# Performance work log

Measured on AMD Instinct MI355X. Metric: run time of the kernel, lower is better.

The kernel has to match this reference:

```python
import jax, jax.numpy as jnp
import numpy as np

N_MASTER = 100000
N_BOND = 200000
N_GLOB = 5000
E1 = 400000
E2 = 100000
D_IN = 64
D_OUT = 64
H = 4
SLOPE = 0.2  # leaky relu negative slope


def _mlp(x, W0, b0, W1, b1, W2):
    # LinearN with num_fc_layers=3: ELU, ELU, Identity (last layer no bias)
    h = jax.nn.elu(x @ W0 + b0)
    h = jax.nn.elu(h @ W1 + b1)
    return h @ W2  # (N, H*D_OUT)


def setup_inputs() -> dict:
    key = jax.random.key(0)
    ks = jax.random.split(key, 32)
    s = 0.1  # weight scale
    d = {
        "master_feats": jax.random.normal(ks[0], (N_MASTER, D_IN), jnp.float32),
        "bond_feats": jax.random.normal(ks[1], (N_BOND, D_IN), jnp.float32),
        "global_feats": jax.random.normal(ks[2], (N_GLOB, D_IN), jnp.float32),
        "atom_W0": jax.random.normal(ks[3], (D_IN, D_OUT), jnp.float32) * s,
        "atom_b0": jnp.zeros((D_OUT,), jnp.float32),
        "atom_W1": jax.random.normal(ks[4], (D_OUT, D_OUT), jnp.float32) * s,
        "atom_b1": jnp.zeros((D_OUT,), jnp.float32),
        "atom_W2": jax.random.normal(ks[5], (D_OUT, H * D_OUT), jnp.float32) * s,
        "bond_W0": jax.random.normal(ks[6], (D_IN, D_OUT), jnp.float32) * s,
        "bond_b0": jnp.zeros((D_OUT,), jnp.float32),
        "bond_W1": jax.random.normal(ks[7], (D_OUT, D_OUT), jnp.float32) * s,
        "bond_b1": jnp.zeros((D_OUT,), jnp.float32),
        "bond_W2": jax.random.normal(ks[8], (D_OUT, H * D_OUT), jnp.float32) * s,
        "glob_W0": jax.random.normal(ks[9], (D_IN, D_OUT), jnp.float32) * s,
        "glob_b0": jnp.zeros((D_OUT,), jnp.float32),
        "glob_W1": jax.random.normal(ks[10], (D_OUT, D_OUT), jnp.float32) * s,
        "glob_b1": jnp.zeros((D_OUT,), jnp.float32),
        "glob_W2": jax.random.normal(ks[11], (D_OUT, H * D_OUT), jnp.float32) * s,
        "attn_l": jax.random.normal(ks[12], (H, D_OUT), jnp.float32) * s,
        "attn_r": jax.random.normal(ks[13], (H, D_OUT), jnp.float32) * s,
        "e1_src": jax.random.randint(ks[14], (E1,), 0, N_BOND, jnp.int32),
        "e1_dst": jax.random.randint(ks[15], (E1,), 0, N_MASTER, jnp.int32),
        "e2_src": jax.random.randint(ks[16], (E2,), 0, N_GLOB, jnp.int32),
        "e2_dst": jax.random.randint(ks[17], (E2,), 0, N_MASTER, jnp.int32),
    }
    return d


def reference(master_feats, bond_feats, global_feats,
              atom_W0, atom_b0, atom_W1, atom_b1, atom_W2,
              bond_W0, bond_b0, bond_W1, bond_b1, bond_W2,
              glob_W0, glob_b0, glob_W1, glob_b1, glob_W2,
              attn_l, attn_r, e1_src, e1_dst, e2_src, e2_dst):
    # Per-node-type projections to (N, H, D_OUT)
    ft_m = _mlp(master_feats, atom_W0, atom_b0, atom_W1, atom_b1, atom_W2).reshape(N_MASTER, H, D_OUT)
    ft_b = _mlp(bond_feats, bond_W0, bond_b0, bond_W1, bond_b1, bond_W2).reshape(N_BOND, H, D_OUT)
    ft_g = _mlp(global_feats, glob_W0, glob_b0, glob_W1, glob_b1, glob_W2).reshape(N_GLOB, H, D_OUT)

    er = jnp.einsum('nhd,hd->nh', ft_m, attn_r)  # master (dst) scores
    el_b = jnp.einsum('nhd,hd->nh', ft_b, attn_l)
    el_g = jnp.einsum('nhd,hd->nh', ft_g, attn_l)

    # Per-edge logits: u_add_v then leaky relu
    e1 = jax.nn.leaky_relu(el_b[e1_src] + er[e1_dst], negative_slope=SLOPE)  # (E1, H)
    e2 = jax.nn.leaky_relu(el_g[e2_src] + er[e2_dst], negative_slope=SLOPE)  # (E2, H)

    # Joint edge softmax over all incoming edges per master node
    dst_all = jnp.concatenate([e1_dst, e2_dst])  # (E1+E2,)
    e_all = jnp.concatenate([e1, e2], axis=0)    # (E1+E2, H)
    emax = jax.ops.segment_max(e_all, dst_all, num_segments=N_MASTER)  # (N, H)
    ex = jnp.exp(e_all - emax[dst_all])
    esum = jax.ops.segment_sum(ex, dst_all, num_segments=N_MASTER)     # (N, H)
    a = ex / esum[dst_all]                                             # (E, H)

    # Aggregate: u_mul_e, sum per destination master node
    src_ft = jnp.concatenate([ft_b[e1_src], ft_g[e2_src]], axis=0)     # (E, H, D)
    msgs = src_ft * a[:, :, None]
    rst = jax.ops.segment_sum(msgs, dst_all, num_segments=N_MASTER)    # (N, H, D)
    return rst
```

## Files before the change

### kernel.cpp

```cpp
#include <hip/hip_runtime.h>

#define NM 100000
#define NB 200000
#define NG 5000
#define NE1 400000
#define NE2 100000
#define NE (NE1 + NE2)
#define NMP 100004
#define SCAN_BLOCKS 391

typedef __attribute__((ext_vector_type(8))) short bf16x8;
typedef __attribute__((ext_vector_type(4))) short short4v;
typedef __attribute__((ext_vector_type(4))) float f32x4;

__device__ __forceinline__ unsigned short f2bf(float f) {
    unsigned int u = __float_as_uint(f);
    u += 0x7FFFu + ((u >> 16) & 1u);
    return (unsigned short)(u >> 16);
}
__device__ __forceinline__ float bf2f(unsigned short u) {
    return __uint_as_float((unsigned int)u << 16);
}
__device__ __forceinline__ float elu_f(float x) {
    return x > 0.f ? x : __expf(x) - 1.f;
}
__device__ __forceinline__ char* swz(char* base, int j, int byteoff) {
    return base + j * 128 + ((((byteoff >> 4) ^ (j & 7)) << 4) | (byteoff & 15));
}

struct WEnt { const float* W; short* o; int I; int off; };
struct WAll { WEnt e[6]; };

__global__ __launch_bounds__(256) void wprep_all_kernel(WAll a)
{
    const int idx = blockIdx.x * 256 + threadIdx.x;
    #pragma unroll
    for (int j = 5; j >= 0; --j) {
        if (idx >= a.e[j].off) {
            const int local = idx - a.e[j].off;
            const int I = a.e[j].I;
            const int i = local >> 6, k = local & 63;
            a.e[j].o[local] = (short)f2bf(a.e[j].W[k * I + i]);
            break;
        }
    }
}

__global__ __launch_bounds__(256) void wt2prep_kernel(
    const float* __restrict__ W2b, const float* __restrict__ W2g,
    short* __restrict__ wt2)
{
    const int idx = blockIdx.x * 256 + threadIdx.x;
    const int i = idx >> 7, k = idx & 127;
    const float v = (k < 64) ? W2b[(k << 8) + i] : W2g[((k - 64) << 8) + i];
    wt2[idx] = (short)f2bf(v);
}

struct Eff3 { const float* W2[3]; const float* attn[3]; float* eff[3]; };
__global__ __launch_bounds__(256) void eff3_kernel(Eff3 a)
{
    const int b = blockIdx.x;
    const int t = threadIdx.x;
    const int h = t >> 6, k = t & 63;
    const float* wrow = a.W2[b] + (k << 8) + (h << 6);
    const float* arow = a.attn[b] + (h << 6);
    float s = 0.f;
    #pragma unroll 8
    for (int d = 0; d < 64; ++d) s = fmaf(wrow[d], arow[d], s);
    a.eff[b][(h << 6) + k] = s;
}

struct MlpArgs {
    const float* x[3]; int N[3];
    const short* W0t[3]; const float* b0[3];
    const short* W1t[3]; const float* b1[3];
    const float* eff[3];
    float* score[3];
    unsigned short* h2o[3];
    int bstart[3];
};

__global__ __launch_bounds__(256, 4) void mlp2_all_kernel(MlpArgs A)
{
    __shared__ __attribute__((aligned(128))) char ldsA[64 * 128];
    __shared__ __attribute__((aligned(128))) char ldsB[64 * 128];

    const int which = (blockIdx.x >= (unsigned)A.bstart[2]) ? 2
                    : (blockIdx.x >= (unsigned)A.bstart[1]) ? 1 : 0;
    const float* x = A.x[which];
    const int N = A.N[which];
    const short* W0t = A.W0t[which];
    const float* b0p = A.b0[which];
    const short* W1t = A.W1t[which];
    const float* b1p = A.b1[which];
    const float* eff = A.eff[which];
    float* score = A.score[which];
    unsigned short* h2p = A.h2o[which];

    const int tid = threadIdx.x;
    const int w = tid >> 6, l = tid & 63;
    const int g = l >> 4, c = l & 15;
    const int r0 = (blockIdx.x - A.bstart[which]) << 6;

    {
        const int j = tid >> 2, q = tid & 3;
        const int row = r0 + j;
        bf16x8 o0 = (bf16x8)0, o1 = (bf16x8)0;
        if (row < N) {
            const float4* xp = (const float4*)(x + ((size_t)row << 6) + (q << 4));
            #pragma unroll
            for (int u = 0; u < 2; ++u) {
                float4 v = xp[u];
                o0[u*4+0] = (short)f2bf(v.x); o0[u*4+1] = (short)f2bf(v.y);
                o0[u*4+2] = (short)f2bf(v.z); o0[u*4+3] = (short)f2bf(v.w);
            }
            #pragma unroll
            for (int u = 0; u < 2; ++u) {
                float4 v = xp[u + 2];
                o1[u*4+0] = (short)f2bf(v.x); o1[u*4+1] = (short)f2bf(v.y);
                o1[u*4+2] = (short)f2bf(v.z); o1[u*4+3] = (short)f2bf(v.w);
            }
        }
        *(bf16x8*)swz(ldsA, j, q * 32)      = o0;
        *(bf16x8*)swz(ldsA, j, q * 32 + 16) = o1;
    }
    __syncthreads();

    char* src = ldsA;
    char* dst = ldsB;
    #pragma unroll
    for (int layer = 0; layer < 2; ++layer) {
        const short* Wt = layer ? W1t : W0t;
        const float* bb = layer ? b1p : b0p;
        f32x4 acc[4] = {};
        #pragma unroll
        for (int step = 0; step < 2; ++step) {
            bf16x8 a = *(const bf16x8*)(Wt + (((16 * w + c) << 6) + 32 * step + 8 * g));
            #pragma unroll
            for (int t = 0; t < 4; ++t) {
                const int j = 16 * t + c;
                bf16x8 b = *(const bf16x8*)swz(src, j, 64 * step + 16 * g);
                acc[t] = __builtin_amdgcn_mfma_f32_16x16x32_bf16(a, b, acc[t], 0, 0, 0);
            }
        }
        const int i0 = 16 * w + 4 * g;
        const float4 bias = *(const float4*)(bb + i0);
        #pragma unroll
        for (int t = 0; t < 4; ++t) {
            const int j = 16 * t + c;
            short4v o;
            o[0] = (short)f2bf(elu_f(acc[t][0] + bias.x));
            o[1] = (short)f2bf(elu_f(acc[t][1] + bias.y));
            o[2] = (short)f2bf(elu_f(acc[t][2] + bias.z));
            o[3] = (short)f2bf(elu_f(acc[t][3] + bias.w));
            *(short4v*)swz(dst, j, 32 * w + 8 * g) = o;
        }
        __syncthreads();
        char* tmp = src; src = dst; dst = tmp;
    }

    {
        const int j = tid >> 2, h = tid & 3;
        const int row = r0 + j;
        float s = 0.f;
        #pragma unroll
        for (int c8 = 0; c8 < 8; ++c8) {
            bf16x8 v = *(const bf16x8*)swz(src, j, c8 * 16);
            const float4 e0 = *(const float4*)(eff + (h << 6) + (c8 << 3));
            const float4 e1 = *(const float4*)(eff + (h << 6) + (c8 << 3) + 4);
            s += bf2f((unsigned short)v[0]) * e0.x + bf2f((unsigned short)v[1]) * e0.y
               + bf2f((unsigned short)v[2]) * e0.z + bf2f((unsigned short)v[3]) * e0.w
               + bf2f((unsigned short)v[4]) * e1.x + bf2f((unsigned short)v[5]) * e1.y
               + bf2f((unsigned short)v[6]) * e1.z + bf2f((unsigned short)v[7]) * e1.w;
        }
        if (row < N) score[(row << 2) + h] = s;
    }

    if (h2p) {
        const int j = tid >> 2, q = tid & 3;
        const int row = r0 + j;
        if (row < N) {
            bf16x8 v0 = *(const bf16x8*)swz(src, j, q * 32);
            bf16x8 v1 = *(const bf16x8*)swz(src, j, q * 32 + 16);
            unsigned short* p = h2p + ((size_t)row << 6) + (q << 4);
            *(bf16x8*)p       = v0;
            *(bf16x8*)(p + 8) = v1;
        }
    }
}

__global__ void hist_kernel(const int* __restrict__ e1_dst,
                            const int* __restrict__ e2_dst,
                            int* __restrict__ counts)
{
    int i = blockIdx.x * blockDim.x + threadIdx.x;
    if (i < NE1) atomicAdd(&counts[e1_dst[i]], 1);
    else if (i < NE) atomicAdd(&counts[e2_dst[i - NE1]], 1);
}

__global__ __launch_bounds__(256) void scan1_kernel(
    const int* __restrict__ counts,
    int* __restrict__ prefix_inc,
    int* __restrict__ blocksums)
{
    const int i = blockIdx.x * 256 + threadIdx.x;
    const int lane = threadIdx.x & 63, wv = threadIdx.x >> 6;
    int v = (i < NM) ? counts[i] : 0;
    int x = v;
    #pragma unroll
    for (int o = 1; o < 64; o <<= 1) {
        int u = __shfl_up(x, o);
        if (lane >= o) x += u;
    }
    __shared__ int wsum[4];
    if (lane == 63) wsum[wv] = x;
    __syncthreads();
    int add = 0;
    #pragma unroll
    for (int k = 0; k < 3; ++k) add += (k < wv) ? wsum[k] : 0;
    x += add;
    if (i < NM) prefix_inc[i] = x;
    if (threadIdx.x == 255) blocksums[blockIdx.x] = x;
}

__global__ __launch_bounds__(512) void scan2_kernel(int* __restrict__ blocksums)
{
    const int t = threadIdx.x;
    const int lane = t & 63, wv = t >> 6;
    int v = (t < SCAN_BLOCKS) ? blocksums[t] : 0;
    int x = v;
    #pragma unroll
    for (int o = 1; o < 64; o <<= 1) {
        int u = __shfl_up(x, o);
        if (lane >= o) x += u;
    }
    __shared__ int wsum[8];
    if (lane == 63) wsum[wv] = x;
    __syncthreads();
    int add = 0;
    #pragma unroll
    for (int k = 0; k < 7; ++k) add += (k < wv) ? wsum[k] : 0;
    x += add;
    if (t < SCAN_BLOCKS) blocksums[t] = x - v;
}

__global__ __launch_bounds__(256) void scan3_kernel(
    const int* __restrict__ counts,
    const int* __restrict__ prefix_inc,
    const int* __restrict__ blocksums,
    int* __restrict__ offsets,
    int* __restrict__ cursor,
    int* __restrict__ cursor2)
{
    const int i = blockIdx.x * 256 + threadIdx.x;
    if (i > NM) return;
    if (i == NM) { offsets[NM] = NE; return; }
    const int off = prefix_inc[i] - counts[i] + blocksums[blockIdx.x];
    offsets[i] = off;
    cursor[i]  = off;
    cursor2[i] = off + counts[i];
}

__global__ void fill_kernel(const int* __restrict__ e1_src,
                            const int* __restrict__ e1_dst,
                            const int* __restrict__ e2_src,
                            const int* __restrict__ e2_dst,
                            const float* __restrict__ er,
                            const float* __restrict__ el_b,
                            const float* __restrict__ el_g,
                            int* __restrict__ cursor,
                            int* __restrict__ cursor2,
                            int* __restrict__ rows,
                            float4* __restrict__ expv)
{
    int i = blockIdx.x * blockDim.x + threadIdx.x;
    if (i >= NE) return;
    int dst, src, row, isglob;
    const float* el;
    if (i < NE1) { src = e1_src[i]; dst = e1_dst[i]; row = src;      el = el_b; isglob = 0; }
    else { int j = i - NE1; src = e2_src[j]; dst = e2_dst[j]; row = NB + src; el = el_g; isglob = 1; }
    const float4 l4 = *(const float4*)(el + (src << 2));
    const float4 r4 = *(const float4*)(er + (dst << 2));
    float4 v;
    v.x = l4.x + r4.x; v.x = v.x > 0.f ? v.x : 0.2f * v.x;
    v.y = l4.y + r4.y; v.y = v.y > 0.f ? v.y : 0.2f * v.y;
    v.z = l4.z + r4.z; v.z = v.z > 0.f ? v.z : 0.2f * v.z;
    v.w = l4.w + r4.w; v.w = v.w > 0.f ? v.w : 0.2f * v.w;
    float4 ev;
    ev.x = __expf(v.x); ev.y = __expf(v.y); ev.z = __expf(v.z); ev.w = __expf(v.w);
    int p = isglob ? (atomicSub(&cursor2[dst], 1) - 1)
                   : atomicAdd(&cursor[dst], 1);
    rows[p] = row;
    expv[p] = ev;
}

#define AGSTR 304
__global__ __launch_bounds__(256) void aggregate_fused_kernel(
    const int* __restrict__ offsets,
    const int* __restrict__ split,
    const int* __restrict__ rows,
    const float* __restrict__ expv,
    const unsigned short* __restrict__ h2,
    const short* __restrict__ wt2,
    float* __restrict__ out)
{
    __shared__ __attribute__((aligned(16))) char agg_lds[64 * AGSTR];

    const int tid = threadIdx.x;
    const int w = tid >> 6, l = tid & 63;
    const int h = l >> 4, c = l & 15;
    const int n0 = blockIdx.x << 4;

    #pragma unroll
    for (int j = 0; j < 4; ++j) {
        const int ln = 4 * w + j;
        const int n  = n0 + ln;
        const int start = offsets[n];
        const int sp    = split[n];
        const int end   = offsets[n + 1];

        f32x4 acc = {}, accg = {};
        float s = 0.f;

        for (int b = start; b < sp; b += 4) {
            float  wg[4];
            short4v gv[4];
            #pragma unroll
            for (int i = 0; i < 4; ++i) {
                const int sl = b + i;
                const int sc = sl < sp ? sl : sp - 1;
                const float wv = expv[(sc << 2) + h];
                wg[i] = (sl < sp) ? wv : 0.f;
                const int row = rows[sc];
                gv[i] = *(const short4v*)(h2 + ((size_t)row << 6) + (c << 2));
            }
            #pragma unroll
            for (int i = 0; i < 4; ++i) {
                s += wg[i];
                acc[0] = fmaf(bf2f((unsigned short)gv[i][0]), wg[i], acc[0]);
                acc[1] = fmaf(bf2f((unsigned short)gv[i][1]), wg[i], acc[1]);
                acc[2] = fmaf(bf2f((unsigned short)gv[i][2]), wg[i], acc[2]);
                acc[3] = fmaf(bf2f((unsigned short)gv[i][3]), wg[i], acc[3]);
            }
        }
        for (int b = sp; b < end; b += 4) {
            float  wg[4];
            short4v gv[4];
            #pragma unroll
            for (int i = 0; i < 4; ++i) {
                const int sl = b + i;
                const int sc = sl < end ? sl : end - 1;
                const float wv = expv[(sc << 2) + h];
                wg[i] = (sl < end) ? wv : 0.f;
                const int row = rows[sc];
                gv[i] = *(const short4v*)(h2 + ((size_t)row << 6) + (c << 2));
            }
            #pragma unroll
            for (int i = 0; i < 4; ++i) {
                s += wg[i];
                accg[0] = fmaf(bf2f((unsigned short)gv[i][0]), wg[i], accg[0]);
                accg[1] = fmaf(bf2f((unsigned short)gv[i][1]), wg[i], accg[1]);
                accg[2] = fmaf(bf2f((unsigned short)gv[i][2]), wg[i], accg[2]);
                accg[3] = fmaf(bf2f((unsigned short)gv[i][3]), wg[i], accg[3]);
            }
        }

        const float inv = (end > start) ? 1.f / s : 0.f;
        char* p = agg_lds + (h * 16 + ln) * AGSTR;
        short4v ob, og;
        ob[0] = (short)f2bf(acc[0] * inv);  ob[1] = (short)f2bf(acc[1] * inv);
        ob[2] = (short)f2bf(acc[2] * inv);  ob[3] = (short)f2bf(acc[3] * inv);
        og[0] = (short)f2bf(accg[0] * inv); og[1] = (short)f2bf(accg[1] * inv);
        og[2] = (short)f2bf(accg[2] * inv); og[3] = (short)f2bf(accg[3] * inv);
        *(short4v*)(p + 8 * c)       = ob;
        *(short4v*)(p + 128 + 8 * c) = og;
    }
    __syncthreads();

    {
        const int g = l >> 4;
        #pragma unroll
        for (int it = 0; it < 4; ++it) {
            f32x4 oacc = {};
            #pragma unroll
            for (int st = 0; st < 4; ++st) {
                bf16x8 a = *(const bf16x8*)(wt2 + ((((w << 6) + (it << 4) + c) << 7) + 32 * st + 8 * g));
                bf16x8 bfrag = *(const bf16x8*)(agg_lds + (w * 16 + c) * AGSTR + 64 * st + 16 * g);
                oacc = __builtin_amdgcn_mfma_f32_16x16x32_bf16(a, bfrag, oacc, 0, 0, 0);
            }
            *(f32x4*)(out + ((size_t)(n0 + c) << 8) + (w << 6) + (it << 4) + (g << 2)) = oacc;
        }
    }
}

extern "C" void kernel_launch(void* const* d_in, const int* in_sizes, int n_in,
                              void* d_out, int out_size, void* d_ws, size_t ws_size,
                              hipStream_t stream)
{
    const float* master = (const float*)d_in[0];
    const float* bond   = (const float*)d_in[1];
    const float* glob   = (const float*)d_in[2];
    const float* aW0 = (const float*)d_in[3];
    const float* ab0 = (const float*)d_in[4];
    const float* aW1 = (const float*)d_in[5];
    const float* ab1 = (const float*)d_in[6];
    const float* aW2 = (const float*)d_in[7];
    const float* bW0 = (const float*)d_in[8];
    const float* bb0 = (const float*)d_in[9];
    const float* bW1 = (const float*)d_in[10];
    const float* bb1 = (const float*)d_in[11];
    const float* bW2 = (const float*)d_in[12];
    const float* gW0 = (const float*)d_in[13];
    const float* gb0 = (const float*)d_in[14];
    const float* gW1 = (const float*)d_in[15];
    const float* gb1 = (const float*)d_in[16];
    const float* gW2 = (const float*)d_in[17];
    const float* attn_l = (const float*)d_in[18];
    const float* attn_r = (const float*)d_in[19];
    const int* e1_src = (const int*)d_in[20];
    const int* e1_dst = (const int*)d_in[21];
    const int* e2_src = (const int*)d_in[22];
    const int* e2_dst = (const int*)d_in[23];
    float* out = (float*)d_out;

    unsigned short* h2 = (unsigned short*)d_ws;
    float* er   = (float*)(h2 + (size_t)(NB + NG) * 64);
    float* el_b = er + (size_t)NM * 4;
    float* el_g = el_b + (size_t)NB * 4;
    int* counts  = (int*)(el_g + (size_t)NG * 4);
    int* offsets = counts + NMP;
    int* cursor  = offsets + NMP;
    int* cursor2 = cursor + NMP;
    int* rows    = cursor2 + NMP;
    float4* expv = (float4*)(rows + NE + 16);
    int* prefix_inc = (int*)(expv + NE);
    int* blocksums  = prefix_inc + NMP;
    float* effR  = (float*)(blocksums + 512);
    float* effLB = effR + 256;
    float* effLG = effLB + 256;
    short* wt2 = (short*)(effLG + 256);
    short* wtA = wt2 + 32768;
    short* wtB = wtA + 8192;
    short* wtG = wtB + 8192;

    hipMemsetAsync(counts, 0, sizeof(int) * NM, stream);

    WAll wa;
    wa.e[0] = {aW0, wtA,         64,     0};
    wa.e[1] = {aW1, wtA + 4096,  64,  4096};
    wa.e[2] = {bW0, wtB,         64,  8192};
    wa.e[3] = {bW1, wtB + 4096,  64, 12288};
    wa.e[4] = {gW0, wtG,         64, 16384};
    wa.e[5] = {gW1, wtG + 4096,  64, 20480};
    wprep_all_kernel<<<96, 256, 0, stream>>>(wa);
    wt2prep_kernel<<<128, 256, 0, stream>>>(bW2, gW2, wt2);
    Eff3 ef;
    ef.W2[0] = aW2; ef.attn[0] = attn_r; ef.eff[0] = effR;
    ef.W2[1] = bW2; ef.attn[1] = attn_l; ef.eff[1] = effLB;
    ef.W2[2] = gW2; ef.attn[2] = attn_l; ef.eff[2] = effLG;
    eff3_kernel<<<3, 256, 0, stream>>>(ef);

    MlpArgs ma;
    ma.x[0] = bond;   ma.N[0] = NB; ma.W0t[0] = wtB; ma.b0[0] = bb0;
    ma.W1t[0] = wtB + 4096; ma.b1[0] = bb1; ma.eff[0] = effLB;
    ma.score[0] = el_b; ma.h2o[0] = h2;
    ma.x[1] = glob;   ma.N[1] = NG; ma.W0t[1] = wtG; ma.b0[1] = gb0;
    ma.W1t[1] = wtG + 4096; ma.b1[1] = gb1; ma.eff[1] = effLG;
    ma.score[1] = el_g; ma.h2o[1] = h2 + (size_t)NB * 64;
    ma.x[2] = master; ma.N[2] = NM; ma.W0t[2] = wtA; ma.b0[2] = ab0;
    ma.W1t[2] = wtA + 4096; ma.b1[2] = ab1; ma.eff[2] = effR;
    ma.score[2] = er;   ma.h2o[2] = nullptr;
    ma.bstart[0] = 0;
    ma.bstart[1] = (NB + 63) / 64;
    ma.bstart[2] = ma.bstart[1] + (NG + 63) / 64;
    const int nblk = ma.bstart[2] + (NM + 63) / 64;
    mlp2_all_kernel<<<nblk, 256, 0, stream>>>(ma);

    hist_kernel<<<(NE + 255) / 256, 256, 0, stream>>>(e1_dst, e2_dst, counts);
    scan1_kernel<<<SCAN_BLOCKS, 256, 0, stream>>>(counts, prefix_inc, blocksums);
    scan2_kernel<<<1, 512, 0, stream>>>(blocksums);
    scan3_kernel<<<SCAN_BLOCKS + 1, 256, 0, stream>>>(counts, prefix_inc, blocksums,
                                                      offsets, cursor, cursor2);
    fill_kernel<<<(NE + 255) / 256, 256, 0, stream>>>(e1_src, e1_dst, e2_src, e2_dst,
                                                      er, el_b, el_g,
                                                      cursor, cursor2, rows, expv);
    aggregate_fused_kernel<<<NM / 16, 256, 0, stream>>>(offsets, cursor2, rows,
                                                        (const float*)expv,
                                                        h2, wt2, out);
}
```

Baseline: 227.7 us.

## Interleave per-node edge gathers in aggregate kernel and raise MLP occupancy bound

The aggregate kernel used to walk the four destination nodes of each wave one after another, each with separate bond and global loops. It now walks all four nodes in lockstep over a shared round count and issues 16 gathers per round, so more memory loads are in flight at once. Each edge's weight is masked into either the bond or the global accumulator, which doubles the FMAs and the register use, and nodes with uneven degrees waste slots. The MLP kernel's launch bounds change from 4 to 6 waves per SIMD, which may force register spills, and the counts memset now also clears the padding entries.

```diff
diff --git a/kernel.cpp b/kernel.cpp
--- a/kernel.cpp
+++ b/kernel.cpp
@@ -80,7 +80,7 @@
     int bstart[3];
 };
 
-__global__ __launch_bounds__(256, 4) void mlp2_all_kernel(MlpArgs A)
+__global__ __launch_bounds__(256, 6) void mlp2_all_kernel(MlpArgs A)
 {
     __shared__ __attribute__((aligned(128))) char ldsA[64 * 128];
     __shared__ __attribute__((aligned(128))) char ldsB[64 * 128];
@@ -311,67 +311,69 @@
     const int h = l >> 4, c = l & 15;
     const int n0 = blockIdx.x << 4;
 
+    int st[4], sp4[4], en[4];
+    #pragma unroll
+    for (int j = 0; j < 4; ++j) {
+        const int n = n0 + 4 * w + j;
+        st[j]  = offsets[n];
+        sp4[j] = split[n];
+        en[j]  = offsets[n + 1];
+    }
+    int rmax = 0;
+    #pragma unroll
+    for (int j = 0; j < 4; ++j) rmax = max(rmax, (en[j] - st[j] + 3) >> 2);
+
+    f32x4 acc[4] = {}, accg[4] = {};
+    float s[4] = {0.f, 0.f, 0.f, 0.f};
+
+    for (int r = 0; r < rmax; ++r) {
+        short4v gv[4][4];
+        float   wb[4][4], wg[4][4];
+        #pragma unroll
+        for (int j = 0; j < 4; ++j) {
+            const int base = st[j] + 4 * r;
+            #pragma unroll
+            for (int i = 0; i < 4; ++i) {
+                const int slot = base + i;
+                const int sc = min(slot, NE - 1);
+                const float wv = expv[(sc << 2) + h];
+                wb[j][i] = (slot < sp4[j]) ? wv : 0.f;
+                wg[j][i] = (slot >= sp4[j] && slot < en[j]) ? wv : 0.f;
+                const int row = rows[sc];
+                gv[j][i] = *(const short4v*)(h2 + ((size_t)row << 6) + (c << 2));
+            }
+        }
+        #pragma unroll
+        for (int j = 0; j < 4; ++j) {
+            #pragma unroll
+            for (int i = 0; i < 4; ++i) {
+                s[j] += wb[j][i] + wg[j][i];
+                const float f0 = bf2f((unsigned short)gv[j][i][0]);
+                const float f1 = bf2f((unsigned short)gv[j][i][1]);
+                const float f2 = bf2f((unsigned short)gv[j][i][2]);
+                const float f3 = bf2f((unsigned short)gv[j][i][3]);
+                acc[j][0]  = fmaf(f0, wb[j][i], acc[j][0]);
+                acc[j][1]  = fmaf(f1, wb[j][i], acc[j][1]);
+                acc[j][2]  = fmaf(f2, wb[j][i], acc[j][2]);
+                acc[j][3]  = fmaf(f3, wb[j][i], acc[j][3]);
+                accg[j][0] = fmaf(f0, wg[j][i], accg[j][0]);
+                accg[j][1] = fmaf(f1, wg[j][i], accg[j][1]);
+                accg[j][2] = fmaf(f2, wg[j][i], accg[j][2]);
+                accg[j][3] = fmaf(f3, wg[j][i], accg[j][3]);
+            }
+        }
+    }
+
     #pragma unroll
     for (int j = 0; j < 4; ++j) {
         const int ln = 4 * w + j;
-        const int n  = n0 + ln;
-        const int start = offsets[n];
-        const int sp    = split[n];
-        const int end   = offsets[n + 1];
-
-        f32x4 acc = {}, accg = {};
-        float s = 0.f;
-
-        for (int b = start; b < sp; b += 4) {
-            float  wg[4];
-            short4v gv[4];
-            #pragma unroll
-            for (int i = 0; i < 4; ++i) {
-                const int sl = b + i;
-                const int sc = sl < sp ? sl : sp - 1;
-                const float wv = expv[(sc << 2) + h];
-                wg[i] = (sl < sp) ? wv : 0.f;
-                const int row = rows[sc];
-                gv[i] = *(const short4v*)(h2 + ((size_t)row << 6) + (c << 2));
-            }
-            #pragma unroll
-            for (int i = 0; i < 4; ++i) {
-                s += wg[i];
-                acc[0] = fmaf(bf2f((unsigned short)gv[i][0]), wg[i], acc[0]);
-                acc[1] = fmaf(bf2f((unsigned short)gv[i][1]), wg[i], acc[1]);
-                acc[2] = fmaf(bf2f((unsigned short)gv[i][2]), wg[i], acc[2]);
-                acc[3] = fmaf(bf2f((unsigned short)gv[i][3]), wg[i], acc[3]);
-            }
-        }
-        for (int b = sp; b < end; b += 4) {
-            float  wg[4];
-            short4v gv[4];
-            #pragma unroll
-            for (int i = 0; i < 4; ++i) {
-                const int sl = b + i;
-                const int sc = sl < end ? sl : end - 1;
-                const float wv = expv[(sc << 2) + h];
-                wg[i] = (sl < end) ? wv : 0.f;
-                const int row = rows[sc];
-                gv[i] = *(const short4v*)(h2 + ((size_t)row << 6) + (c << 2));
-            }
-            #pragma unroll
-            for (int i = 0; i < 4; ++i) {
-                s += wg[i];
-                accg[0] = fmaf(bf2f((unsigned short)gv[i][0]), wg[i], accg[0]);
-                accg[1] = fmaf(bf2f((unsigned short)gv[i][1]), wg[i], accg[1]);
-                accg[2] = fmaf(bf2f((unsigned short)gv[i][2]), wg[i], accg[2]);
-                accg[3] = fmaf(bf2f((unsigned short)gv[i][3]), wg[i], accg[3]);
-            }
-        }
-
-        const float inv = (end > start) ? 1.f / s : 0.f;
+        const float inv = (en[j] > st[j]) ? 1.f / s[j] : 0.f;
         char* p = agg_lds + (h * 16 + ln) * AGSTR;
         short4v ob, og;
-        ob[0] = (short)f2bf(acc[0] * inv);  ob[1] = (short)f2bf(acc[1] * inv);
-        ob[2] = (short)f2bf(acc[2] * inv);  ob[3] = (short)f2bf(acc[3] * inv);
-        og[0] = (short)f2bf(accg[0] * inv); og[1] = (short)f2bf(accg[1] * inv);
-        og[2] = (short)f2bf(accg[2] * inv); og[3] = (short)f2bf(accg[3] * inv);
+        ob[0] = (short)f2bf(acc[j][0] * inv);  ob[1] = (short)f2bf(acc[j][1] * inv);
+        ob[2] = (short)f2bf(acc[j][2] * inv);  ob[3] = (short)f2bf(acc[j][3] * inv);
+        og[0] = (short)f2bf(accg[j][0] * inv); og[1] = (short)f2bf(accg[j][1] * inv);
+        og[2] = (short)f2bf(accg[j][2] * inv); og[3] = (short)f2bf(accg[j][3] * inv);
         *(short4v*)(p + 8 * c)       = ob;
         *(short4v*)(p + 128 + 8 * c) = og;
     }
@@ -383,9 +385,9 @@
         for (int it = 0; it < 4; ++it) {
             f32x4 oacc = {};
             #pragma unroll
-            for (int st = 0; st < 4; ++st) {
-                bf16x8 a = *(const bf16x8*)(wt2 + ((((w << 6) + (it << 4) + c) << 7) + 32 * st + 8 * g));
-                bf16x8 bfrag = *(const bf16x8*)(agg_lds + (w * 16 + c) * AGSTR + 64 * st + 16 * g);
+            for (int stp = 0; stp < 4; ++stp) {
+                bf16x8 a = *(const bf16x8*)(wt2 + ((((w << 6) + (it << 4) + c) << 7) + 32 * stp + 8 * g));
+                bf16x8 bfrag = *(const bf16x8*)(agg_lds + (w * 16 + c) * AGSTR + 64 * stp + 16 * g);
                 oacc = __builtin_amdgcn_mfma_f32_16x16x32_bf16(a, bfrag, oacc, 0, 0, 0);
             }
             *(f32x4*)(out + ((size_t)(n0 + c) << 8) + (w << 6) + (it << 4) + (g << 2)) = oacc;
@@ -443,7 +445,7 @@
     short* wtB = wtA + 8192;
     short* wtG = wtB + 8192;
 
-    hipMemsetAsync(counts, 0, sizeof(int) * NM, stream);
+    hipMemsetAsync(counts, 0, sizeof(int) * NMP, stream);
 
     WAll wa;
     wa.e[0] = {aW0, wtA,         64,     0};
```

Result: slower. 293.1 us (+28.7%).
